# Kernel optimization log

Hardware: AMD Instinct MI355X
Metric: run time of the kernel (lower is better)

## Reference

```python
import jax, jax.numpy as jnp
import numpy as np

NUM_LABELS = 64  # number of distinct label ids (0 = background, unchanged)


def setup_inputs() -> dict:
    key = jax.random.key(0)
    k1, k2, k3 = jax.random.split(key, 3)
    shape = (2, 192, 256, 256)
    texturized = jax.random.normal(k1, shape, dtype=jnp.float32)
    label_map = jax.random.randint(k2, shape, 0, NUM_LABELS, dtype=jnp.int32)
    # one Uniform(0, intensity) draw per label, mirroring self.intensity() per loop iter
    intensities = jax.random.uniform(k3, (NUM_LABELS,), dtype=jnp.float32)
    return {"texturized": texturized, "label_map": label_map, "intensities": intensities}


def reference(texturized, label_map, intensities):
    # Per label l > 0 (torch loop): adjusted[mask_l] -= mean(tex[mask_l] - intensity_l)
    #                             = tex - (segment_mean_l - intensity_l) on mask_l.
    flat_tex = texturized.reshape(-1)
    flat_lab = label_map.reshape(-1)
    sums = jax.ops.segment_sum(flat_tex, flat_lab, num_segments=NUM_LABELS)
    counts = jax.ops.segment_sum(jnp.ones_like(flat_tex), flat_lab, num_segments=NUM_LABELS)
    means = sums / jnp.maximum(counts, 1.0)
    delta = means - intensities  # [NUM_LABELS] per-label bls.mean()
    adj = flat_tex - jnp.where(flat_lab > 0, delta[flat_lab], 0.0)
    return adj.reshape(texturized.shape)
```

## Files before the change

kernel.cpp:

```cpp
#include <hip/hip_runtime.h>

#define NUM_LABELS 64
#define NWAVES 4

__global__ __launch_bounds__(256) void tl_reduce(const float* __restrict__ tex,
                                                 const int* __restrict__ lab,
                                                 float* __restrict__ g_sums,
                                                 unsigned int* __restrict__ g_cnts,
                                                 int n) {
    __shared__ float s_sum[NWAVES][NUM_LABELS];
    __shared__ unsigned int s_cnt[NWAVES][NUM_LABELS];
    const int wave = threadIdx.x >> 6;

    for (int i = threadIdx.x; i < NWAVES * NUM_LABELS; i += 256) {
        (&s_sum[0][0])[i] = 0.0f;
        (&s_cnt[0][0])[i] = 0u;
    }
    __syncthreads();

    const int n4 = n >> 2;
    const float4* __restrict__ tex4 = (const float4*)tex;
    const int4* __restrict__ lab4 = (const int4*)lab;
    const int stride = gridDim.x * blockDim.x;

    for (int i = blockIdx.x * blockDim.x + threadIdx.x; i < n4; i += stride) {
        float4 t = tex4[i];
        int4 l = lab4[i];
        atomicAdd(&s_sum[wave][l.x], t.x); atomicAdd(&s_cnt[wave][l.x], 1u);
        atomicAdd(&s_sum[wave][l.y], t.y); atomicAdd(&s_cnt[wave][l.y], 1u);
        atomicAdd(&s_sum[wave][l.z], t.z); atomicAdd(&s_cnt[wave][l.z], 1u);
        atomicAdd(&s_sum[wave][l.w], t.w); atomicAdd(&s_cnt[wave][l.w], 1u);
    }

    if (blockIdx.x == 0) {
        int base = n4 << 2;
        int rem = n - base;
        if ((int)threadIdx.x < rem) {
            int i = base + threadIdx.x;
            atomicAdd(&s_sum[wave][lab[i]], tex[i]);
            atomicAdd(&s_cnt[wave][lab[i]], 1u);
        }
    }
    __syncthreads();

    for (int l = threadIdx.x; l < NUM_LABELS; l += 256) {
        float s = 0.0f;
        unsigned int c = 0u;
        for (int w = 0; w < NWAVES; ++w) { s += s_sum[w][l]; c += s_cnt[w][l]; }
        if (c) {
            atomicAdd(&g_sums[l], s);
            atomicAdd(&g_cnts[l], c);
        }
    }
}

__global__ __launch_bounds__(256) void tl_apply(const float* __restrict__ tex,
                                                const int* __restrict__ lab,
                                                const float* __restrict__ g_sums,
                                                const unsigned int* __restrict__ g_cnts,
                                                const float* __restrict__ intens,
                                                float* __restrict__ out, int n) {
    __shared__ float s_delta[NUM_LABELS];
    if (threadIdx.x < NUM_LABELS) {
        int l = threadIdx.x;
        float c = (float)g_cnts[l];
        float mean = g_sums[l] / fmaxf(c, 1.0f);
        s_delta[l] = (l > 0) ? (mean - intens[l]) : 0.0f;
    }
    __syncthreads();

    const int n4 = n >> 2;
    int i = blockIdx.x * blockDim.x + threadIdx.x;
    if (i < n4) {
        float4 t = ((const float4*)tex)[i];
        int4 l = ((const int4*)lab)[i];
        float4 o;
        o.x = t.x - s_delta[l.x & (NUM_LABELS - 1)];
        o.y = t.y - s_delta[l.y & (NUM_LABELS - 1)];
        o.z = t.z - s_delta[l.z & (NUM_LABELS - 1)];
        o.w = t.w - s_delta[l.w & (NUM_LABELS - 1)];
        ((float4*)out)[i] = o;
    }
    if (blockIdx.x == 0) {
        int base = n4 << 2;
        int rem = n - base;
        if ((int)threadIdx.x < rem) {
            int j = base + threadIdx.x;
            out[j] = tex[j] - s_delta[lab[j] & (NUM_LABELS - 1)];
        }
    }
}

extern "C" void kernel_launch(void* const* d_in, const int* in_sizes, int n_in,
                              void* d_out, int out_size, void* d_ws, size_t ws_size,
                              hipStream_t stream) {
    const float* tex    = (const float*)d_in[0];
    const int*   lab    = (const int*)d_in[1];
    const float* intens = (const float*)d_in[2];
    float* out = (float*)d_out;
    const int n = in_sizes[0];

    float* g_sums = (float*)d_ws;
    unsigned int* g_cnts = (unsigned int*)((char*)d_ws + NUM_LABELS * sizeof(float));

    hipMemsetAsync(d_ws, 0, NUM_LABELS * (sizeof(float) + sizeof(unsigned int)), stream);

    tl_reduce<<<2048, 256, 0, stream>>>(tex, lab, g_sums, g_cnts, n);

    const int n4 = n >> 2;
    const int blocks = (n4 + 255) / 256;
    tl_apply<<<blocks, 256, 0, stream>>>(tex, lab, g_sums, g_cnts, intens, out, n);
}
```

Before: 341.7 us.

## Replace shared-memory atomics with per-lane private label histograms in reduce

The reduce kernel moves from per-wave shared atomics to one-wave blocks where each lane owns its own column of a 64x64 sum and count histogram. Plain read-modify-write updates replace LDS atomics, and the next float4 pair is prefetched in software. A transposed, rotated column sum then produces one global atomic per label per block. Counts become floats, which can lose exactness once a per-lane count passes 2^24 (not reached at these sizes). Occupancy drops to 64-thread blocks using 32KB of LDS each.

```diff
diff --git a/kernel.cpp b/kernel.cpp
--- a/kernel.cpp
+++ b/kernel.cpp
@@ -1,92 +1,103 @@
 #include <hip/hip_runtime.h>
 
-#define NUM_LABELS 64
-#define NWAVES 4
+#define NL 64
 
-__global__ __launch_bounds__(256) void tl_reduce(const float* __restrict__ tex,
-                                                 const int* __restrict__ lab,
-                                                 float* __restrict__ g_sums,
-                                                 unsigned int* __restrict__ g_cnts,
-                                                 int n) {
-    __shared__ float s_sum[NWAVES][NUM_LABELS];
-    __shared__ unsigned int s_cnt[NWAVES][NUM_LABELS];
-    const int wave = threadIdx.x >> 6;
+__global__ __launch_bounds__(64) void tl_reduce(const float* __restrict__ tex,
+                                                const int* __restrict__ lab,
+                                                float* __restrict__ g_sums,
+                                                float* __restrict__ g_cnts,
+                                                int n) {
+    __shared__ float s_sum[NL][NL];
+    __shared__ float s_cnt[NL][NL];
+    const int lane = threadIdx.x;
 
-    for (int i = threadIdx.x; i < NWAVES * NUM_LABELS; i += 256) {
-        (&s_sum[0][0])[i] = 0.0f;
-        (&s_cnt[0][0])[i] = 0u;
+    float4 z = make_float4(0.f, 0.f, 0.f, 0.f);
+    float4* ps = (float4*)&s_sum[0][0];
+    float4* pc = (float4*)&s_cnt[0][0];
+    #pragma unroll
+    for (int i = 0; i < (NL * NL / 4) / NL; ++i) {
+        ps[i * NL + lane] = z;
+        pc[i * NL + lane] = z;
     }
     __syncthreads();
 
     const int n4 = n >> 2;
     const float4* __restrict__ tex4 = (const float4*)tex;
     const int4* __restrict__ lab4 = (const int4*)lab;
-    const int stride = gridDim.x * blockDim.x;
+    const int stride = gridDim.x * NL;
 
-    for (int i = blockIdx.x * blockDim.x + threadIdx.x; i < n4; i += stride) {
-        float4 t = tex4[i];
-        int4 l = lab4[i];
-        atomicAdd(&s_sum[wave][l.x], t.x); atomicAdd(&s_cnt[wave][l.x], 1u);
-        atomicAdd(&s_sum[wave][l.y], t.y); atomicAdd(&s_cnt[wave][l.y], 1u);
-        atomicAdd(&s_sum[wave][l.z], t.z); atomicAdd(&s_cnt[wave][l.z], 1u);
-        atomicAdd(&s_sum[wave][l.w], t.w); atomicAdd(&s_cnt[wave][l.w], 1u);
+    int i = blockIdx.x * NL + lane;
+    bool valid = i < n4;
+    float4 t; int4 l;
+    if (valid) { t = tex4[i]; l = lab4[i]; }
+    while (valid) {
+        const int inext = i + stride;
+        const bool vnext = inext < n4;
+        float4 tn; int4 ln;
+        if (vnext) { tn = tex4[inext]; ln = lab4[inext]; }
+
+        s_sum[l.x & (NL - 1)][lane] += t.x;  s_cnt[l.x & (NL - 1)][lane] += 1.0f;
+        s_sum[l.y & (NL - 1)][lane] += t.y;  s_cnt[l.y & (NL - 1)][lane] += 1.0f;
+        s_sum[l.z & (NL - 1)][lane] += t.z;  s_cnt[l.z & (NL - 1)][lane] += 1.0f;
+        s_sum[l.w & (NL - 1)][lane] += t.w;  s_cnt[l.w & (NL - 1)][lane] += 1.0f;
+
+        i = inext; valid = vnext; t = tn; l = ln;
     }
 
     if (blockIdx.x == 0) {
-        int base = n4 << 2;
-        int rem = n - base;
-        if ((int)threadIdx.x < rem) {
-            int i = base + threadIdx.x;
-            atomicAdd(&s_sum[wave][lab[i]], tex[i]);
-            atomicAdd(&s_cnt[wave][lab[i]], 1u);
+        const int base = n4 << 2;
+        const int rem = n - base;
+        if (lane < rem) {
+            const int j = base + lane;
+            s_sum[lab[j] & (NL - 1)][lane] += tex[j];
+            s_cnt[lab[j] & (NL - 1)][lane] += 1.0f;
         }
     }
     __syncthreads();
 
-    for (int l = threadIdx.x; l < NUM_LABELS; l += 256) {
-        float s = 0.0f;
-        unsigned int c = 0u;
-        for (int w = 0; w < NWAVES; ++w) { s += s_sum[w][l]; c += s_cnt[w][l]; }
-        if (c) {
-            atomicAdd(&g_sums[l], s);
-            atomicAdd(&g_cnts[l], c);
-        }
+    float s = 0.f, c = 0.f;
+    #pragma unroll
+    for (int k = 0; k < NL; ++k) {
+        const int col = (k + lane) & (NL - 1);
+        s += s_sum[lane][col];
+        c += s_cnt[lane][col];
     }
+    atomicAdd(&g_sums[lane], s);
+    atomicAdd(&g_cnts[lane], c);
 }
 
 __global__ __launch_bounds__(256) void tl_apply(const float* __restrict__ tex,
                                                 const int* __restrict__ lab,
                                                 const float* __restrict__ g_sums,
-                                                const unsigned int* __restrict__ g_cnts,
+                                                const float* __restrict__ g_cnts,
                                                 const float* __restrict__ intens,
                                                 float* __restrict__ out, int n) {
-    __shared__ float s_delta[NUM_LABELS];
-    if (threadIdx.x < NUM_LABELS) {
-        int l = threadIdx.x;
-        float c = (float)g_cnts[l];
-        float mean = g_sums[l] / fmaxf(c, 1.0f);
+    __shared__ float s_delta[NL];
+    if (threadIdx.x < NL) {
+        const int l = threadIdx.x;
+        const float mean = g_sums[l] / fmaxf(g_cnts[l], 1.0f);
         s_delta[l] = (l > 0) ? (mean - intens[l]) : 0.0f;
     }
     __syncthreads();
 
     const int n4 = n >> 2;
-    int i = blockIdx.x * blockDim.x + threadIdx.x;
+    const int i = blockIdx.x * blockDim.x + threadIdx.x;
     if (i < n4) {
-        float4 t = ((const float4*)tex)[i];
-        int4 l = ((const int4*)lab)[i];
+        const float4 t = ((const float4*)tex)[i];
+        const int4 l = ((const int4*)lab)[i];
         float4 o;
-        o.x = t.x - s_delta[l.x & (NUM_LABELS - 1)];
-        o.y = t.y - s_delta[l.y & (NUM_LABELS - 1)];
-        o.z = t.z - s_delta[l.z & (NUM_LABELS - 1)];
-        o.w = t.w - s_delta[l.w & (NUM_LABELS - 1)];
+        o.x = t.x - s_delta[l.x & (NL - 1)];
+        o.y = t.y - s_delta[l.y & (NL - 1)];
+        o.z = t.z - s_delta[l.z & (NL - 1)];
+        o.w = t.w - s_delta[l.w & (NL - 1)];
         ((float4*)out)[i] = o;
     }
     if (blockIdx.x == 0) {
-        int base = n4 << 2;
-        int rem = n - base;
+        const int base = n4 << 2;
+        const int rem = n - base;
         if ((int)threadIdx.x < rem) {
-            int j = base + threadIdx.x;
-            out[j] = tex[j] - s_delta[lab[j] & (NUM_LABELS - 1)];
+            const int j = base + threadIdx.x;
+            out[j] = tex[j] - s_delta[lab[j] & (NL - 1)];
         }
     }
 }
@@ -101,11 +112,11 @@
     const int n = in_sizes[0];
 
     float* g_sums = (float*)d_ws;
-    unsigned int* g_cnts = (unsigned int*)((char*)d_ws + NUM_LABELS * sizeof(float));
+    float* g_cnts = (float*)((char*)d_ws + NL * sizeof(float));
 
-    hipMemsetAsync(d_ws, 0, NUM_LABELS * (sizeof(float) + sizeof(unsigned int)), stream);
+    hipMemsetAsync(d_ws, 0, 2 * NL * sizeof(float), stream);
 
-    tl_reduce<<<2048, 256, 0, stream>>>(tex, lab, g_sums, g_cnts, n);
+    tl_reduce<<<1280, NL, 0, stream>>>(tex, lab, g_sums, g_cnts, n);
 
     const int n4 = n >> 2;
     const int blocks = (n4 + 255) / 256;
```

After: 354.0 us. 1.04x slower.
